# Optimization experiments

Measured on AMD Instinct MI355X. Metric: run time of the kernel, lower is better.

The kernel has to match this reference:

```python
import jax, jax.numpy as jnp
from jax import lax
import numpy as np

GLOVE_VOCAB, GLOVE_DIM = 400000, 300
CHAR_VOCAB, CHAR_EMB, CHAR_HID = 100, 50, 128
N_WORDS, WORD_LEN = 4096, 16
HIDDEN, OUT = 512, 2


def setup_inputs() -> dict:
    key = jax.random.key(0)
    ks = jax.random.split(key, 12)
    s = 0.02
    return {
        "word_indices": jax.random.randint(ks[0], (N_WORDS,), 0, GLOVE_VOCAB),
        "char_indices": jax.random.randint(ks[1], (N_WORDS, WORD_LEN), 0, CHAR_VOCAB),
        "glove_table": jax.random.normal(ks[2], (GLOVE_VOCAB, GLOVE_DIM), jnp.float32) * s,
        "char_embed": jax.random.normal(ks[3], (CHAR_VOCAB, CHAR_EMB), jnp.float32) * s,
        "W_ih": jax.random.normal(ks[4], (4 * CHAR_HID, CHAR_EMB), jnp.float32) * s,
        "W_hh": jax.random.normal(ks[5], (4 * CHAR_HID, CHAR_HID), jnp.float32) * s,
        "b_ih": jnp.zeros((4 * CHAR_HID,), jnp.float32),
        "b_hh": jnp.zeros((4 * CHAR_HID,), jnp.float32),
        "fc1_w": jax.random.normal(ks[6], (HIDDEN, GLOVE_DIM + CHAR_HID), jnp.float32) * s,
        "fc1_b": jnp.zeros((HIDDEN,), jnp.float32),
        "fc2_w": jax.random.normal(ks[7], (OUT, HIDDEN), jnp.float32) * s,
        "fc2_b": jnp.zeros((OUT,), jnp.float32),
    }


def _char_lstm(ch_emb, W_ih, W_hh, b_ih, b_hh):
    # ch_emb: [N, L, E] -> final hidden [N, H]. Batched over all words at once
    # (replaces the per-word Python loop in the torch module).
    N = ch_emb.shape[0]
    H = W_hh.shape[1]
    b = b_ih + b_hh

    def step(carry, x_t):
        h, c = carry
        gates = x_t @ W_ih.T + h @ W_hh.T + b  # [N, 4H]
        i, f, g, o = jnp.split(gates, 4, axis=-1)
        c = jax.nn.sigmoid(f) * c + jax.nn.sigmoid(i) * jnp.tanh(g)
        h = jax.nn.sigmoid(o) * jnp.tanh(c)
        return (h, c), None

    h0 = jnp.zeros((N, H), ch_emb.dtype)
    (h, _), _ = lax.scan(step, (h0, h0), jnp.swapaxes(ch_emb, 0, 1))
    return h


def reference(word_indices, char_indices, glove_table, char_embed,
              W_ih, W_hh, b_ih, b_hh, fc1_w, fc1_b, fc2_w, fc2_b):
    glove = glove_table[word_indices]          # [N, D] fused embedding gather
    ch = char_embed[char_indices]              # [N, L, E]
    char_h = _char_lstm(ch, W_ih, W_hh, b_ih, b_hh)  # [N, H]
    hybrid = jnp.concatenate([glove, char_h], axis=-1)  # [N, D+H]
    avg = jnp.mean(hybrid, axis=0)[None, :]    # [1, D+H] (deep-averaging)
    # dropout is identity in eval mode
    hid = jax.nn.relu(avg @ fc1_w.T + fc1_b)
    return hid @ fc2_w.T + fc2_b               # [1, OUT] logits
```

## Files before the change

### kernel.cpp

```cpp
#include <hip/hip_runtime.h>
#include <hip/hip_bf16.h>
#include <math.h>

#define NW        4096
#define WLEN      16
#define CEMB      50
#define CHID      128
#define NGATE     512
#define GDIM      300
#define FEAT      428
#define NHID      512
#define CVOCAB    100
#define NBLK      256


typedef __attribute__((ext_vector_type(8))) short bf16x8;
typedef __attribute__((ext_vector_type(4))) float f32x4;

__device__ __forceinline__ unsigned short f2bf(float x) {
    __hip_bfloat16 h = __float2bfloat16(x);
    return __builtin_bit_cast(unsigned short, h);
}
__device__ __forceinline__ float bf2f(unsigned short u) {
    unsigned int v = ((unsigned int)u) << 16;
    return __builtin_bit_cast(float, v);
}
__device__ __forceinline__ float sigmoid_f(float x) { return 1.f / (1.f + expf(-x)); }

__global__ void glove_sum_kernel(const int* __restrict__ word_idx,
                                 const float* __restrict__ glove,
                                 float* __restrict__ gpart) {
    const int tid = threadIdx.x;
    const int b = blockIdx.x;
    const int wbase = b * 16;
    float acc0 = 0.f, acc1 = 0.f;
#pragma unroll
    for (int w = 0; w < 16; ++w) {
        const int row = word_idx[wbase + w];
        const float* r = glove + (size_t)row * GDIM;
        if (tid < GDIM) acc0 += r[tid];
        if (tid + 256 < GDIM) acc1 += r[tid + 256];
    }
    if (tid < GDIM) gpart[b * 304 + tid] = acc0;
    if (tid + 256 < GDIM) gpart[b * 304 + tid + 256] = acc1;
}

__global__ void inproj_kernel(const float* __restrict__ char_embed,
                              const float* __restrict__ W_ih,
                              const float* __restrict__ b_ih,
                              const float* __restrict__ b_hh,
                              float* __restrict__ P) {
    __shared__ float slab[128 * 51];
    __shared__ float ce[CEMB];
    const int c = blockIdx.x >> 2, jt = blockIdx.x & 3;
    const int t = threadIdx.x;
    for (int s = t; s < 128 * CEMB; s += 128) {
        const int j = s / CEMB, e = s - j * CEMB;
        slab[j * 51 + e] = W_ih[jt * (128 * CEMB) + s];
    }
    if (t < CEMB) ce[t] = char_embed[c * CEMB + t];
    __syncthreads();
    const int g = jt * 128 + t;
    float acc = b_ih[g] + b_hh[g];
#pragma unroll
    for (int e = 0; e < CEMB; ++e) acc = fmaf(ce[e], slab[t * 51 + e], acc);
    P[c * NGATE + g] = acc;
}

__global__ __launch_bounds__(512, 2)
void lstm_kernel(const int* __restrict__ char_idx,
                 const float* __restrict__ Whh,
                 const float* __restrict__ P,
                 float* __restrict__ cpart) {
    __shared__ __align__(16) unsigned short Hh[16 * 128];
    __shared__ __align__(16) unsigned short Hl[16 * 128];
    __shared__ int ci[16][17];
    const int t = threadIdx.x;
    const int wm = t >> 6, lane = t & 63;
    const int w = lane & 15, hi = lane >> 4;

    bf16x8 ah[4][4], al[4][4];
#pragma unroll
    for (int r = 0; r < 4; ++r) {
        const int g = (wm + 8 * r) * 16 + (lane & 15);
        const float* wp = Whh + g * CHID + hi * 8;
#pragma unroll
        for (int ks = 0; ks < 4; ++ks) {
            union { bf16x8 v; unsigned short u[8]; } ph, pl;
#pragma unroll
            for (int j = 0; j < 8; ++j) {
                const float x = wp[ks * 32 + j];
                const unsigned short xh = f2bf(x);
                ph.u[j] = xh;
                pl.u[j] = f2bf(x - bf2f(xh));
            }
            ah[r][ks] = ph.v;
            al[r][ks] = pl.v;
        }
    }

    const int wbase = blockIdx.x * 16;
    if (t < 256) ci[t >> 4][t & 15] = char_idx[(wbase + (t >> 4)) * WLEN + (t & 15)];

    {
        unsigned int* hz = (unsigned int*)Hh;
        hz[t] = 0u; hz[t + 512] = 0u;
        unsigned int* lz = (unsigned int*)Hl;
        lz[t] = 0u; lz[t + 512] = 0u;
    }

    float cst[4] = {0.f, 0.f, 0.f, 0.f};
    float hreg[4] = {0.f, 0.f, 0.f, 0.f};
    __syncthreads();

    for (int s = 0; s < WLEN; ++s) {
        const int cix = ci[w][s];
        const float* prow = P + cix * NGATE + wm * 16 + hi * 4;
        f32x4 pv[4];
#pragma unroll
        for (int r = 0; r < 4; ++r) pv[r] = *(const f32x4*)(prow + r * 128);

        bf16x8 bh[4], bl[4];
#pragma unroll
        for (int ks = 0; ks < 4; ++ks) {
            const int chunk = (ks * 4 + hi) ^ w;
            bh[ks] = *(const bf16x8*)((const char*)Hh + w * 256 + chunk * 16);
            bl[ks] = *(const bf16x8*)((const char*)Hl + w * 256 + chunk * 16);
        }

        f32x4 d[4];
#pragma unroll
        for (int r = 0; r < 4; ++r) d[r] = (f32x4){0.f, 0.f, 0.f, 0.f};
#pragma unroll
        for (int ks = 0; ks < 4; ++ks)
#pragma unroll
            for (int r = 0; r < 4; ++r)
                d[r] = __builtin_amdgcn_mfma_f32_16x16x32_bf16(ah[r][ks], bh[ks], d[r], 0, 0, 0);
#pragma unroll
        for (int ks = 0; ks < 4; ++ks)
#pragma unroll
            for (int r = 0; r < 4; ++r)
                d[r] = __builtin_amdgcn_mfma_f32_16x16x32_bf16(al[r][ks], bh[ks], d[r], 0, 0, 0);
#pragma unroll
        for (int ks = 0; ks < 4; ++ks)
#pragma unroll
            for (int r = 0; r < 4; ++r)
                d[r] = __builtin_amdgcn_mfma_f32_16x16x32_bf16(ah[r][ks], bl[ks], d[r], 0, 0, 0);
        __syncthreads();

#pragma unroll
        for (int reg = 0; reg < 4; ++reg) {
            const float ig = d[0][reg] + pv[0][reg];
            const float fg = d[1][reg] + pv[1][reg];
            const float gg = d[2][reg] + pv[2][reg];
            const float og = d[3][reg] + pv[3][reg];
            const float si = sigmoid_f(ig);
            const float sf = sigmoid_f(fg);
            const float so = sigmoid_f(og);
            cst[reg] = sf * cst[reg] + si * tanhf(gg);
            const float hv = so * tanhf(cst[reg]);
            hreg[reg] = hv;
            const int n = wm * 16 + hi * 4 + reg;
            const int idx = w * 128 + (((n >> 3) ^ w) << 3) + (n & 7);
            const unsigned short hh16 = f2bf(hv);
            Hh[idx] = hh16;
            Hl[idx] = f2bf(hv - bf2f(hh16));
        }
        __syncthreads();
    }

#pragma unroll
    for (int reg = 0; reg < 4; ++reg) {
        float v = hreg[reg];
#pragma unroll
        for (int m = 1; m < 16; m <<= 1) v += __shfl_xor(v, m);
        if ((lane & 15) == 0)
            cpart[blockIdx.x * CHID + wm * 16 + hi * 4 + reg] = v;
    }
}

__global__ void reduce_kernel(const float* __restrict__ gpart,
                              const float* __restrict__ cpart,
                              float* __restrict__ sums) {
    const int t = threadIdx.x;
    if (t >= FEAT) return;
    float a0 = 0.f, a1 = 0.f, a2 = 0.f, a3 = 0.f;
    if (t < GDIM) {
        for (int b = 0; b < NBLK; b += 4) {
            a0 += gpart[(b + 0) * 304 + t];
            a1 += gpart[(b + 1) * 304 + t];
            a2 += gpart[(b + 2) * 304 + t];
            a3 += gpart[(b + 3) * 304 + t];
        }
    } else {
        const int n = t - GDIM;
        for (int b = 0; b < NBLK; b += 4) {
            a0 += cpart[(b + 0) * CHID + n];
            a1 += cpart[(b + 1) * CHID + n];
            a2 += cpart[(b + 2) * CHID + n];
            a3 += cpart[(b + 3) * CHID + n];
        }
    }
    sums[t] = (a0 + a1) + (a2 + a3);
}

__global__ void fc1_kernel(const float* __restrict__ fc1_w,
                           const float* __restrict__ fc1_b,
                           const float* __restrict__ sums,
                           float* __restrict__ hid) {
    __shared__ __align__(16) float avg[FEAT];
    const int t = threadIdx.x;
    if (t < FEAT) avg[t] = sums[t] * (1.f / (float)NW);
    __syncthreads();

    const int wave = t >> 6, lane = t & 63;
    const int half = lane >> 5, lane32 = lane & 31;
    const int r = blockIdx.x * 16 + wave * 2 + half;

    float acc = 0.f;
    const float* row = fc1_w + (size_t)r * FEAT;
#pragma unroll
    for (int i = 0; i < 4; ++i) {
        const int c0 = i * 128 + lane32 * 4;
        if (c0 + 4 <= FEAT) {
            const f32x4 wv = *(const f32x4*)(row + c0);
            const f32x4 av = *(const f32x4*)(avg + c0);
            acc = fmaf(av[0], wv[0], acc);
            acc = fmaf(av[1], wv[1], acc);
            acc = fmaf(av[2], wv[2], acc);
            acc = fmaf(av[3], wv[3], acc);
        }
    }
#pragma unroll
    for (int m = 1; m < 32; m <<= 1) acc += __shfl_xor(acc, m);
    if (lane32 == 0) hid[r] = fmaxf(acc + fc1_b[r], 0.f);
}

__global__ void fc2_kernel(const float* __restrict__ fc2_w,
                           const float* __restrict__ fc2_b,
                           const float* __restrict__ hid,
                           float* __restrict__ out) {
    const int t = threadIdx.x;
    const int r = t >> 6, lane = t & 63;
    float p = 0.f;
#pragma unroll
    for (int i = 0; i < 8; ++i)
        p = fmaf(hid[i * 64 + lane], fc2_w[r * NHID + i * 64 + lane], p);
#pragma unroll
    for (int off = 32; off > 0; off >>= 1) p += __shfl_down(p, off);
    if (lane == 0) out[r] = p + fc2_b[r];
}

extern "C" void kernel_launch(void* const* d_in, const int* in_sizes, int n_in,
                              void* d_out, int out_size, void* d_ws, size_t ws_size,
                              hipStream_t stream) {
    const int*   word_idx   = (const int*)d_in[0];
    const int*   char_idx   = (const int*)d_in[1];
    const float* glove      = (const float*)d_in[2];
    const float* char_embed = (const float*)d_in[3];
    const float* W_ih       = (const float*)d_in[4];
    const float* W_hh       = (const float*)d_in[5];
    const float* b_ih       = (const float*)d_in[6];
    const float* b_hh       = (const float*)d_in[7];
    const float* fc1_w      = (const float*)d_in[8];
    const float* fc1_b      = (const float*)d_in[9];
    const float* fc2_w      = (const float*)d_in[10];
    const float* fc2_b      = (const float*)d_in[11];
    float* out = (float*)d_out;
    float* ws  = (float*)d_ws;

    float* sums  = ws;
    float* P     = ws + 512;
    float* hid   = ws + 51712;
    float* gpart = ws + 52224;
    float* cpart = ws + 130048;

    inproj_kernel<<<400, 128, 0, stream>>>(char_embed, W_ih, b_ih, b_hh, P);
    glove_sum_kernel<<<NBLK, 256, 0, stream>>>(word_idx, glove, gpart);
    lstm_kernel<<<NBLK, 512, 0, stream>>>(char_idx, W_hh, P, cpart);
    reduce_kernel<<<1, 512, 0, stream>>>(gpart, cpart, sums);
    fc1_kernel<<<32, 512, 0, stream>>>(fc1_w, fc1_b, sums, hid);
    fc2_kernel<<<1, 128, 0, stream>>>(fc2_w, fc2_b, hid, out);
}
```

Baseline: 616.4 us.

## Fuse embedding kernels, double-buffer LSTM hidden state, merge reduce into fc1

Combines the input-projection and GloVe gather-sum into one launch that splits work by block index. It also merges the partial-sum reduction into the fc1 kernel, so each of its 32 blocks redoes the reduction. The LSTM hidden-state buffers in shared memory are now double-buffered, which removes one __syncthreads per timestep. The cost is extra shared memory, redundant reduction work across the fc1 blocks, and uncoalesced per-thread W_ih row reads in the projection.

After: 605.7 us. About the same (-1.7%).

```diff
diff --git a/kernel.cpp b/kernel.cpp
--- a/kernel.cpp
+++ b/kernel.cpp
@@ -27,44 +27,40 @@
 }
 __device__ __forceinline__ float sigmoid_f(float x) { return 1.f / (1.f + expf(-x)); }
 
-__global__ void glove_sum_kernel(const int* __restrict__ word_idx,
-                                 const float* __restrict__ glove,
-                                 float* __restrict__ gpart) {
-    const int tid = threadIdx.x;
-    const int b = blockIdx.x;
-    const int wbase = b * 16;
-    float acc0 = 0.f, acc1 = 0.f;
-#pragma unroll
-    for (int w = 0; w < 16; ++w) {
-        const int row = word_idx[wbase + w];
-        const float* r = glove + (size_t)row * GDIM;
-        if (tid < GDIM) acc0 += r[tid];
-        if (tid + 256 < GDIM) acc1 += r[tid + 256];
-    }
-    if (tid < GDIM) gpart[b * 304 + tid] = acc0;
-    if (tid + 256 < GDIM) gpart[b * 304 + tid + 256] = acc1;
-}
-
-__global__ void inproj_kernel(const float* __restrict__ char_embed,
-                              const float* __restrict__ W_ih,
-                              const float* __restrict__ b_ih,
-                              const float* __restrict__ b_hh,
-                              float* __restrict__ P) {
-    __shared__ float slab[128 * 51];
-    __shared__ float ce[CEMB];
-    const int c = blockIdx.x >> 2, jt = blockIdx.x & 3;
-    const int t = threadIdx.x;
-    for (int s = t; s < 128 * CEMB; s += 128) {
-        const int j = s / CEMB, e = s - j * CEMB;
-        slab[j * 51 + e] = W_ih[jt * (128 * CEMB) + s];
-    }
-    if (t < CEMB) ce[t] = char_embed[c * CEMB + t];
-    __syncthreads();
-    const int g = jt * 128 + t;
-    float acc = b_ih[g] + b_hh[g];
-#pragma unroll
-    for (int e = 0; e < CEMB; ++e) acc = fmaf(ce[e], slab[t * 51 + e], acc);
-    P[c * NGATE + g] = acc;
+__global__ void fused_embed_kernel(const int* __restrict__ word_idx,
+                                   const float* __restrict__ glove,
+                                   const float* __restrict__ char_embed,
+                                   const float* __restrict__ W_ih,
+                                   const float* __restrict__ b_ih,
+                                   const float* __restrict__ b_hh,
+                                   float* __restrict__ P,
+                                   float* __restrict__ gpart) {
+    const int bid = blockIdx.x, t = threadIdx.x;
+    if (bid < 200) {
+        __shared__ float ce[CEMB];
+        const int c = bid >> 1;
+        const int g = (bid & 1) * 256 + t;
+        if (t < CEMB) ce[t] = char_embed[c * CEMB + t];
+        __syncthreads();
+        float acc = b_ih[g] + b_hh[g];
+        const float* wrow = W_ih + g * CEMB;
+#pragma unroll
+        for (int e = 0; e < CEMB; ++e) acc = fmaf(ce[e], wrow[e], acc);
+        P[c * NGATE + g] = acc;
+    } else {
+        const int b = bid - 200;
+        const int wbase = b * 16;
+        float acc0 = 0.f, acc1 = 0.f;
+#pragma unroll
+        for (int w = 0; w < 16; ++w) {
+            const int row = word_idx[wbase + w];
+            const float* r = glove + (size_t)row * GDIM;
+            if (t < GDIM) acc0 += r[t];
+            if (t + 256 < GDIM) acc1 += r[t + 256];
+        }
+        if (t < GDIM) gpart[b * 304 + t] = acc0;
+        if (t + 256 < GDIM) gpart[b * 304 + t + 256] = acc1;
+    }
 }
 
 __global__ __launch_bounds__(512, 2)
@@ -72,8 +68,8 @@
                  const float* __restrict__ Whh,
                  const float* __restrict__ P,
                  float* __restrict__ cpart) {
-    __shared__ __align__(16) unsigned short Hh[16 * 128];
-    __shared__ __align__(16) unsigned short Hl[16 * 128];
+    __shared__ __align__(16) unsigned short Hh[2][16 * 128];
+    __shared__ __align__(16) unsigned short Hl[2][16 * 128];
     __shared__ int ci[16][17];
     const int t = threadIdx.x;
     const int wm = t >> 6, lane = t & 63;
@@ -103,9 +99,9 @@
     if (t < 256) ci[t >> 4][t & 15] = char_idx[(wbase + (t >> 4)) * WLEN + (t & 15)];
 
     {
-        unsigned int* hz = (unsigned int*)Hh;
+        unsigned int* hz = (unsigned int*)&Hh[0][0];
         hz[t] = 0u; hz[t + 512] = 0u;
-        unsigned int* lz = (unsigned int*)Hl;
+        unsigned int* lz = (unsigned int*)&Hl[0][0];
         lz[t] = 0u; lz[t + 512] = 0u;
     }
 
@@ -114,6 +110,8 @@
     __syncthreads();
 
     for (int s = 0; s < WLEN; ++s) {
+        const int cur = s & 1, nxt = cur ^ 1;
+
         const int cix = ci[w][s];
         const float* prow = P + cix * NGATE + wm * 16 + hi * 4;
         f32x4 pv[4];
@@ -124,8 +122,8 @@
 #pragma unroll
         for (int ks = 0; ks < 4; ++ks) {
             const int chunk = (ks * 4 + hi) ^ w;
-            bh[ks] = *(const bf16x8*)((const char*)Hh + w * 256 + chunk * 16);
-            bl[ks] = *(const bf16x8*)((const char*)Hl + w * 256 + chunk * 16);
+            bh[ks] = *(const bf16x8*)((const char*)&Hh[cur][0] + w * 256 + chunk * 16);
+            bl[ks] = *(const bf16x8*)((const char*)&Hl[cur][0] + w * 256 + chunk * 16);
         }
 
         f32x4 d[4];
@@ -146,7 +144,6 @@
 #pragma unroll
             for (int r = 0; r < 4; ++r)
                 d[r] = __builtin_amdgcn_mfma_f32_16x16x32_bf16(ah[r][ks], bl[ks], d[r], 0, 0, 0);
-        __syncthreads();
 
 #pragma unroll
         for (int reg = 0; reg < 4; ++reg) {
@@ -163,8 +160,8 @@
             const int n = wm * 16 + hi * 4 + reg;
             const int idx = w * 128 + (((n >> 3) ^ w) << 3) + (n & 7);
             const unsigned short hh16 = f2bf(hv);
-            Hh[idx] = hh16;
-            Hl[idx] = f2bf(hv - bf2f(hh16));
+            Hh[nxt][idx] = hh16;
+            Hl[nxt][idx] = f2bf(hv - bf2f(hh16));
         }
         __syncthreads();
     }
@@ -179,38 +176,33 @@
     }
 }
 
-__global__ void reduce_kernel(const float* __restrict__ gpart,
-                              const float* __restrict__ cpart,
-                              float* __restrict__ sums) {
-    const int t = threadIdx.x;
-    if (t >= FEAT) return;
-    float a0 = 0.f, a1 = 0.f, a2 = 0.f, a3 = 0.f;
-    if (t < GDIM) {
-        for (int b = 0; b < NBLK; b += 4) {
-            a0 += gpart[(b + 0) * 304 + t];
-            a1 += gpart[(b + 1) * 304 + t];
-            a2 += gpart[(b + 2) * 304 + t];
-            a3 += gpart[(b + 3) * 304 + t];
-        }
-    } else {
-        const int n = t - GDIM;
-        for (int b = 0; b < NBLK; b += 4) {
-            a0 += cpart[(b + 0) * CHID + n];
-            a1 += cpart[(b + 1) * CHID + n];
-            a2 += cpart[(b + 2) * CHID + n];
-            a3 += cpart[(b + 3) * CHID + n];
-        }
-    }
-    sums[t] = (a0 + a1) + (a2 + a3);
-}
-
-__global__ void fc1_kernel(const float* __restrict__ fc1_w,
-                           const float* __restrict__ fc1_b,
-                           const float* __restrict__ sums,
-                           float* __restrict__ hid) {
+__global__ void tail_kernel(const float* __restrict__ gpart,
+                            const float* __restrict__ cpart,
+                            const float* __restrict__ fc1_w,
+                            const float* __restrict__ fc1_b,
+                            float* __restrict__ hid) {
     __shared__ __align__(16) float avg[FEAT];
     const int t = threadIdx.x;
-    if (t < FEAT) avg[t] = sums[t] * (1.f / (float)NW);
+    if (t < FEAT) {
+        float a0 = 0.f, a1 = 0.f, a2 = 0.f, a3 = 0.f;
+        if (t < GDIM) {
+            for (int b = 0; b < NBLK; b += 4) {
+                a0 += gpart[(b + 0) * 304 + t];
+                a1 += gpart[(b + 1) * 304 + t];
+                a2 += gpart[(b + 2) * 304 + t];
+                a3 += gpart[(b + 3) * 304 + t];
+            }
+        } else {
+            const int n = t - GDIM;
+            for (int b = 0; b < NBLK; b += 4) {
+                a0 += cpart[(b + 0) * CHID + n];
+                a1 += cpart[(b + 1) * CHID + n];
+                a2 += cpart[(b + 2) * CHID + n];
+                a3 += cpart[(b + 3) * CHID + n];
+            }
+        }
+        avg[t] = ((a0 + a1) + (a2 + a3)) * (1.f / (float)NW);
+    }
     __syncthreads();
 
     const int wave = t >> 6, lane = t & 63;
@@ -269,16 +261,14 @@
     float* out = (float*)d_out;
     float* ws  = (float*)d_ws;
 
-    float* sums  = ws;
     float* P     = ws + 512;
     float* hid   = ws + 51712;
     float* gpart = ws + 52224;
     float* cpart = ws + 130048;
 
-    inproj_kernel<<<400, 128, 0, stream>>>(char_embed, W_ih, b_ih, b_hh, P);
-    glove_sum_kernel<<<NBLK, 256, 0, stream>>>(word_idx, glove, gpart);
+    fused_embed_kernel<<<456, 256, 0, stream>>>(word_idx, glove, char_embed,
+                                                W_ih, b_ih, b_hh, P, gpart);
     lstm_kernel<<<NBLK, 512, 0, stream>>>(char_idx, W_hh, P, cpart);
-    reduce_kernel<<<1, 512, 0, stream>>>(gpart, cpart, sums);
-    fc1_kernel<<<32, 512, 0, stream>>>(fc1_w, fc1_b, sums, hid);
+    tail_kernel<<<32, 512, 0, stream>>>(gpart, cpart, fc1_w, fc1_b, hid);
     fc2_kernel<<<1, 128, 0, stream>>>(fc2_w, fc2_b, hid, out);
 }
```
